# Performance work log

Measured on AMD Instinct MI355X. Metric: run time of the kernel, lower is better.

## Reference

```python
import jax, jax.numpy as jnp
import numpy as np

B, S_SRC, S_TGT = 32, 128, 128
V, E, H = 32000, 256, 256
PAD_ID = 0
NEG = -1.0e9


def setup_inputs() -> dict:
    key = jax.random.key(0)
    ks = jax.random.split(key, 16)
    lengths_de = jax.random.randint(ks[0], (B,), S_SRC // 2, S_SRC + 1)
    idx_de = jax.random.randint(ks[1], (B, S_SRC), 1, V)
    pos = jnp.arange(S_SRC)[None, :]
    indices_de = jnp.where(pos < lengths_de[:, None], idx_de, PAD_ID)
    indices_en = jax.random.randint(ks[2], (B, S_TGT), 1, V)
    lengths_en = jnp.full((B,), S_TGT, dtype=jnp.int32)

    sc = 0.02
    def nrm(k, shape):
        return jax.random.normal(k, shape, dtype=jnp.float32) * sc
    emb_enc = nrm(ks[3], (V, E)).at[PAD_ID].set(0.0)
    emb_dec = nrm(ks[4], (V, E)).at[PAD_ID].set(0.0)
    return {
        "indices_de": indices_de, "lengths_de": lengths_de,
        "indices_en": indices_en, "lengths_en": lengths_en,
        "emb_enc": emb_enc, "emb_dec": emb_dec,
        "W_ih_enc": nrm(ks[5], (H, E)), "W_hh_enc": nrm(ks[6], (H, H)),
        "b_ih_enc": jnp.zeros((H,), jnp.float32), "b_hh_enc": jnp.zeros((H,), jnp.float32),
        "W_ih_dec": nrm(ks[7], (H, E)), "W_hh_dec": nrm(ks[8], (H, H)),
        "b_ih_dec": jnp.zeros((H,), jnp.float32), "b_hh_dec": jnp.zeros((H,), jnp.float32),
        "W_attn": nrm(ks[9], (H, 2 * H)), "b_attn": jnp.zeros((H,), jnp.float32),
        "W_out": nrm(ks[10], (V, H)), "b_out": jnp.zeros((V,), jnp.float32),
    }


def reference(indices_de, lengths_de, indices_en, lengths_en,
              emb_enc, emb_dec,
              W_ih_enc, W_hh_enc, b_ih_enc, b_hh_enc,
              W_ih_dec, W_hh_dec, b_ih_dec, b_hh_dec,
              W_attn, b_attn, W_out, b_out):
    # ---- Encoder: tanh RNN over packed sequence ----
    x_enc = emb_enc[indices_de]                      # [B, S, E]
    valid = jnp.arange(S_SRC)[None, :] < lengths_de[:, None]  # [B, S]

    def enc_step(h, inp):
        x_t, v_t = inp                                # [B,E], [B]
        h_new = jnp.tanh(x_t @ W_ih_enc.T + b_ih_enc + h @ W_hh_enc.T + b_hh_enc)
        h = jnp.where(v_t[:, None], h_new, h)         # frozen past length (pack semantics)
        out = jnp.where(v_t[:, None], h_new, 0.0)     # padded outputs are zero
        return h, out

    h0 = jnp.zeros((B, H), jnp.float32)
    h_final, enc_outs = jax.lax.scan(
        enc_step, h0, (x_enc.transpose(1, 0, 2), valid.T))
    encoder_outputs = enc_outs.transpose(1, 0, 2)     # [B, S, H]
    enc_mask = indices_de == PAD_ID                   # [B, S] True at padding

    # ---- Decoder: per-step RNN cell + dot-product attention + vocab proj ----
    x_dec = emb_dec[indices_en]                       # [B, T, E]

    def dec_step(h, x_t):
        h = jnp.tanh(x_t @ W_ih_dec.T + b_ih_dec + h @ W_hh_dec.T + b_hh_dec)
        scores = jnp.einsum('bh,bsh->bs', h, encoder_outputs)
        scores = jnp.where(enc_mask, NEG, scores)
        attn = jax.nn.softmax(scores, axis=-1)
        context = jnp.einsum('bs,bsh->bh', attn, encoder_outputs)
        combined = jnp.concatenate([context, h], axis=1)          # [B, 2H]
        attn_out = jnp.tanh(combined @ W_attn.T + b_attn)         # [B, H]
        logits_t = attn_out @ W_out.T + b_out                     # [B, V]
        return h, logits_t

    _, logits = jax.lax.scan(dec_step, h_final, x_dec.transpose(1, 0, 2))
    return logits.transpose(1, 0, 2)                  # [B, T, V]
```

## Files before the change

kernel.cpp:

```cpp
#include <hip/hip_runtime.h>
#include <stdint.h>

#define B_ 32
#define S_ 128
#define T_ 128
#define V_ 32000
#define E_ 256
#define H_ 256
#define NEG_ (-1.0e9f)

typedef __attribute__((ext_vector_type(8))) short short8;
typedef __attribute__((ext_vector_type(4))) float floatx4;

__device__ __forceinline__ unsigned short f2bf(float x){
  unsigned u = __float_as_uint(x);
  u = u + 0x7fffu + ((u >> 16) & 1u);
  return (unsigned short)(u >> 16);
}
__device__ __forceinline__ float bf2f(unsigned short s){
  return __uint_as_float(((unsigned)s) << 16);
}
__device__ __forceinline__ float hsum4(float4 v){ return (v.x+v.y)+(v.z+v.w); }
__device__ __forceinline__ void unpack8(uint4 q, float4& lo, float4& hi){
  lo.x = __uint_as_float(q.x << 16); lo.y = __uint_as_float(q.x & 0xffff0000u);
  lo.z = __uint_as_float(q.y << 16); lo.w = __uint_as_float(q.y & 0xffff0000u);
  hi.x = __uint_as_float(q.z << 16); hi.y = __uint_as_float(q.z & 0xffff0000u);
  hi.z = __uint_as_float(q.w << 16); hi.w = __uint_as_float(q.w & 0xffff0000u);
}

#define GLOAD_LDS16(gptr, lptr) \
  __builtin_amdgcn_global_load_lds( \
      (const __attribute__((address_space(1))) unsigned int*)(const void*)(gptr), \
      (__attribute__((address_space(3))) unsigned int*)(void*)(lptr), 16, 0, 0)

#define LDS_BARRIER() do { \
    asm volatile("s_waitcnt lgkmcnt(0)" ::: "memory"); \
    __builtin_amdgcn_s_barrier(); \
  } while(0)

__device__ __forceinline__ void cvt_body(const float* __restrict__ src,
                                         unsigned short* __restrict__ dst,
                                         int blk, int n4){
  int i = blk*256 + (int)threadIdx.x;
  if (i < n4){
    float4 v = ((const float4*)src)[i];
    ushort4 o; o.x=f2bf(v.x); o.y=f2bf(v.y); o.z=f2bf(v.z); o.w=f2bf(v.w);
    ((ushort4*)dst)[i] = o;
  }
}

__device__ __forceinline__ void xih_body(
    const int* __restrict__ idxmat, const float* __restrict__ emb,
    const float* __restrict__ Wih,
    const float* __restrict__ b1, const float* __restrict__ b2,
    float* __restrict__ out, int blk,
    int* idx_s, float4 (*x_s)[64])
{
  int b = blk >> 3;
  int t0 = (blk & 7) << 4;
  int tid = threadIdx.x;
  if (tid < 16) idx_s[tid] = idxmat[b*128 + t0 + tid];
  __syncthreads();
  for (int r = 0; r < 16; ++r)
    ((float*)&x_s[r][0])[tid] = emb[(size_t)idx_s[r]*E_ + tid];
  __syncthreads();
  int j2 = tid & 127, tg = tid >> 7;
  const float4* W0 = (const float4*)(Wih + (size_t)j2*E_);
  const float4* W1 = (const float4*)(Wih + (size_t)(j2+128)*E_);
  float4 a0[8], a1[8];
  #pragma unroll
  for (int t=0;t<8;++t){ a0[t]={0,0,0,0}; a1[t]={0,0,0,0}; }
  for (int e4 = 0; e4 < 64; ++e4){
    float4 w0 = W0[e4], w1 = W1[e4];
    #pragma unroll
    for (int t = 0; t < 8; ++t){
      float4 xv = x_s[tg*8+t][e4];
      a0[t] += w0*xv; a1[t] += w1*xv;
    }
  }
  float bi0 = b1[j2] + b2[j2];
  float bi1 = b1[j2+128] + b2[j2+128];
  #pragma unroll
  for (int t = 0; t < 8; ++t){
    size_t row = (size_t)((b<<7) + t0 + tg*8 + t)*H_;
    out[row + j2]     = hsum4(a0[t]) + bi0;
    out[row + j2+128] = hsum4(a1[t]) + bi1;
  }
}

__global__ __launch_bounds__(256) void k_prep(
    const float* __restrict__ W_out, unsigned short* __restrict__ Wout_bf,
    const float* __restrict__ W_attn, unsigned short* __restrict__ Wattn_bf,
    const int* __restrict__ indices_de, const float* __restrict__ emb_enc,
    const float* __restrict__ W_ih_enc, const float* __restrict__ b_ih_enc,
    const float* __restrict__ b_hh_enc, float* __restrict__ Xih_enc,
    const int* __restrict__ indices_en, const float* __restrict__ emb_dec,
    const float* __restrict__ W_ih_dec, const float* __restrict__ b_ih_dec,
    const float* __restrict__ b_hh_dec, float* __restrict__ Xih_dec)
{
  __shared__ int idx_s[16];
  __shared__ float4 x_s[16][64];
  int bx = blockIdx.x;
  if (bx < 8000){
    cvt_body(W_out, Wout_bf, bx, 2048000);
  } else if (bx < 8128){
    cvt_body(W_attn, Wattn_bf, bx - 8000, 32768);
  } else if (bx < 8384){
    xih_body(indices_de, emb_enc, W_ih_enc, b_ih_enc, b_hh_enc, Xih_enc,
             bx - 8128, idx_s, x_s);
  } else {
    xih_body(indices_en, emb_dec, W_ih_dec, b_ih_dec, b_hh_dec, Xih_dec,
             bx - 8384, idx_s, x_s);
  }
}

__global__ __launch_bounds__(512, 2) void k_rnn2(
    const float* __restrict__ Whh_e, const float* __restrict__ Whh_d,
    const float* __restrict__ Xih_e, const float* __restrict__ Xih_d,
    const int* __restrict__ lengths,
    unsigned short* __restrict__ enc_out,
    float* __restrict__ hseq)
{
  __shared__ float4 h4_s[64];
  __shared__ float part[2][256];
  float* h_s = (float*)h4_s;
  int b = blockIdx.x, tid = threadIdx.x;
  int j = tid & 255, half = tid >> 8;
  float4 w[32];
  const float4* Wr = (const float4*)(Whh_e + (size_t)j*H_ + half*128);
  #pragma unroll
  for (int i = 0; i < 32; ++i) w[i] = Wr[i];
  if (tid < 256) h_s[tid] = 0.f;
  int len = lengths[b];
  __syncthreads();

  for (int t = 0; t < 128; ++t){
    float x = 0.f;
    if (tid < 256) x = Xih_e[(size_t)((b<<7) + t)*H_ + j];
    const float4* hh = h4_s + (half << 5);
    float4 acc0 = {0,0,0,0}, acc1 = {0,0,0,0};
    #pragma unroll
    for (int i = 0; i < 32; i += 2){ acc0 += w[i]*hh[i]; acc1 += w[i+1]*hh[i+1]; }
    part[half][j] = hsum4(acc0) + hsum4(acc1);
    LDS_BARRIER();
    if (tid < 256){
      float s = x + part[0][tid] + part[1][tid];
      float hn = tanhf(s);
      float hold = h_s[tid];
      bool v = (t < len);
      h_s[tid] = v ? hn : hold;
      enc_out[(size_t)((b<<7)+t)*H_ + tid] = f2bf(v ? hn : 0.f);
    }
    LDS_BARRIER();
  }

  Wr = (const float4*)(Whh_d + (size_t)j*H_ + half*128);
  #pragma unroll
  for (int i = 0; i < 32; ++i) w[i] = Wr[i];
  for (int t = 0; t < 128; ++t){
    float x = 0.f;
    if (tid < 256) x = Xih_d[(size_t)((b<<7) + t)*H_ + j];
    const float4* hh = h4_s + (half << 5);
    float4 acc0 = {0,0,0,0}, acc1 = {0,0,0,0};
    #pragma unroll
    for (int i = 0; i < 32; i += 2){ acc0 += w[i]*hh[i]; acc1 += w[i+1]*hh[i+1]; }
    part[half][j] = hsum4(acc0) + hsum4(acc1);
    LDS_BARRIER();
    if (tid < 256){
      float s = x + part[0][tid] + part[1][tid];
      float hn = tanhf(s);
      h_s[tid] = hn;
      hseq[(size_t)((b<<7)+t)*H_ + tid] = hn;
    }
    LDS_BARRIER();
  }
}

__global__ __launch_bounds__(256) void k_attn(
    const unsigned short* __restrict__ enc_out,
    const float* __restrict__ hseq,
    const int* __restrict__ lengths,
    const unsigned short* __restrict__ Wattn,
    const float* __restrict__ battn,
    unsigned short* __restrict__ attn_out)
{
  __shared__ float h_sm[16][256];
  __shared__ float sc[16][132];
  __shared__ float comb[16][512];
  int bx = blockIdx.x; int b = bx >> 3; int t0 = (bx & 7) << 4;
  int tid = threadIdx.x;
  int len = lengths[b];
  for (int r = 0; r < 16; ++r)
    h_sm[r][tid] = hseq[(size_t)((b<<7) + t0 + r)*H_ + tid];
  __syncthreads();
  {
    int s = tid & 127, tg = tid >> 7;
    float4 a[8];
    #pragma unroll
    for (int t=0;t<8;++t) a[t] = {0,0,0,0};
    const uint4* ep = (const uint4*)(enc_out + (size_t)(b*S_ + s)*H_);
    for (int oct = 0; oct < 32; ++oct){
      uint4 q = ep[oct];
      float4 elo, ehi; unpack8(q, elo, ehi);
      #pragma unroll
      for (int t = 0; t < 8; ++t){
        const float4* hp = (const float4*)&h_sm[tg*8+t][oct*8];
        a[t] += elo*hp[0] + ehi*hp[1];
      }
    }
    #pragma unroll
    for (int t = 0; t < 8; ++t)
      sc[tg*8+t][s] = (s < len) ? hsum4(a[t]) : NEG_;
  }
  __syncthreads();
  {
    int wv = tid >> 6, ln = tid & 63;
    for (int r = 0; r < 4; ++r){
      int t = r*4 + wv;
      float v0 = sc[t][ln], v1 = sc[t][ln+64];
      float m = fmaxf(v0, v1);
      #pragma unroll
      for (int off = 32; off >= 1; off >>= 1) m = fmaxf(m, __shfl_xor(m, off));
      float e0 = __expf(v0 - m), e1 = __expf(v1 - m);
      float su = e0 + e1;
      #pragma unroll
      for (int off = 32; off >= 1; off >>= 1) su += __shfl_xor(su, off);
      float inv = 1.0f / su;
      sc[t][ln] = e0*inv; sc[t][ln+64] = e1*inv;
    }
  }
  __syncthreads();
  {
    int hd = tid & 127, tg = tid >> 7;
    float c0[8], c1[8];
    #pragma unroll
    for (int t=0;t<8;++t){ c0[t]=0.f; c1[t]=0.f; }
    for (int s4 = 0; s4 < 32; ++s4){
      float ea[4], eb[4];
      #pragma unroll
      for (int i = 0; i < 4; ++i){
        const unsigned short* er = enc_out + (size_t)(b*S_ + s4*4 + i)*H_;
        ea[i] = bf2f(er[hd]); eb[i] = bf2f(er[hd+128]);
      }
      #pragma unroll
      for (int t = 0; t < 8; ++t){
        float4 av = *(const float4*)&sc[tg*8+t][s4*4];
        c0[t] += av.x*ea[0] + av.y*ea[1] + av.z*ea[2] + av.w*ea[3];
        c1[t] += av.x*eb[0] + av.y*eb[1] + av.z*eb[2] + av.w*eb[3];
      }
    }
    #pragma unroll
    for (int t = 0; t < 8; ++t){
      comb[tg*8+t][hd]     = c0[t];
      comb[tg*8+t][hd+128] = c1[t];
    }
  }
  for (int r = 0; r < 16; ++r) comb[r][256 + tid] = h_sm[r][tid];
  __syncthreads();
  {
    int j2 = tid & 127, tg = tid >> 7;
    float4 a0[8], a1[8];
    #pragma unroll
    for (int t=0;t<8;++t){ a0[t]={0,0,0,0}; a1[t]={0,0,0,0}; }
    const uint4* W0 = (const uint4*)(Wattn + (size_t)j2*512);
    const uint4* W1 = (const uint4*)(Wattn + (size_t)(j2+128)*512);
    for (int oct = 0; oct < 64; ++oct){
      float4 w0lo, w0hi, w1lo, w1hi;
      unpack8(W0[oct], w0lo, w0hi);
      unpack8(W1[oct], w1lo, w1hi);
      #pragma unroll
      for (int t = 0; t < 8; ++t){
        const float4* cp = (const float4*)&comb[tg*8+t][oct*8];
        float4 clo = cp[0], chi = cp[1];
        a0[t] += w0lo*clo + w0hi*chi;
        a1[t] += w1lo*clo + w1hi*chi;
      }
    }
    float bi0 = battn[j2], bi1 = battn[j2+128];
    #pragma unroll
    for (int t = 0; t < 8; ++t){
      size_t row = (size_t)((b<<7) + t0 + tg*8 + t)*H_;
      attn_out[row + j2]     = f2bf(tanhf(hsum4(a0[t]) + bi0));
      attn_out[row + j2+128] = f2bf(tanhf(hsum4(a1[t]) + bi1));
    }
  }
}

__global__ __launch_bounds__(512) void k_vocab(
    const unsigned short* __restrict__ A,
    const unsigned short* __restrict__ Wb,
    const float* __restrict__ bout,
    float* __restrict__ out)
{
  __shared__ alignas(16) unsigned short Asm[2][256*32];
  __shared__ alignas(16) unsigned short Bsm[2][128*32];
  int bid = blockIdx.x;
  int xcd = bid & 7, idx = bid >> 3;
  int nb = idx >> 1;
  int mb = (xcd << 1) | (idx & 1);
  int tid = threadIdx.x;
  int ln  = tid & 63;
  int wid = tid >> 6;
  int llo = ln & 15, lhi = ln >> 4;
  int wr = wid >> 1, wc = wid & 1;
  int mbase = mb*256, nbase = nb*128;

  int ca0 = tid, ca1 = tid + 512, cb = tid;
  int ra0 = ca0 >> 2, sa0 = (ca0 & 3) ^ ((ra0 >> 1) & 3);
  int ra1 = ca1 >> 2, sa1 = (ca1 & 3) ^ ((ra1 >> 1) & 3);
  int rb  = cb  >> 2, sb  = (cb  & 3) ^ ((rb  >> 1) & 3);
  const unsigned short* Ag0 = A  + (size_t)(mbase + ra0)*256 + sa0*8;
  const unsigned short* Ag1 = A  + (size_t)(mbase + ra1)*256 + sa1*8;
  const unsigned short* Bg  = Wb + (size_t)(nbase + rb )*256 + sb*8;

#define STAGE_V(bufi, kk) do { \
    GLOAD_LDS16(Ag0 + (kk), &Asm[bufi][ca0*8]); \
    GLOAD_LDS16(Ag1 + (kk), &Asm[bufi][ca1*8]); \
    GLOAD_LDS16(Bg  + (kk), &Bsm[bufi][cb*8]); \
  } while(0)

  floatx4 acc[4][4];
  #pragma unroll
  for (int mi=0;mi<4;++mi)
    #pragma unroll
    for (int ni=0;ni<4;++ni) acc[mi][ni] = (floatx4){0.f,0.f,0.f,0.f};

  int q = (llo >> 1) & 3;
  int aoff[4], boff[4];
  #pragma unroll
  for (int i=0;i<4;++i){
    aoff[i] = (wr*64 + i*16 + llo)*32 + ((lhi ^ q)*8);
    boff[i] = (wc*64 + i*16 + llo)*32 + ((lhi ^ q)*8);
  }

  STAGE_V(0, 0);
  asm volatile("s_waitcnt vmcnt(0)" ::: "memory");
  __builtin_amdgcn_s_barrier();

  #pragma unroll
  for (int k0 = 0; k0 < 8; ++k0){
    int cur = k0 & 1;
    if (k0 < 7) STAGE_V(cur^1, (k0+1)*32);
    short8 afr[4];
    #pragma unroll
    for (int mi=0;mi<4;++mi)
      afr[mi] = *(const short8*)&Asm[cur][aoff[mi]];
    #pragma unroll
    for (int ni=0;ni<4;++ni){
      short8 bfr = *(const short8*)&Bsm[cur][boff[ni]];
      #pragma unroll
      for (int mi=0;mi<4;++mi)
        acc[mi][ni] = __builtin_amdgcn_mfma_f32_16x16x32_bf16(afr[mi], bfr, acc[mi][ni], 0, 0, 0);
    }
    asm volatile("s_waitcnt vmcnt(0)" ::: "memory");
    __builtin_amdgcn_s_barrier();
  }

  #pragma unroll
  for (int ni = 0; ni < 4; ++ni){
    int col = nbase + wc*64 + ni*16 + llo;
    float bias = bout[col];
    #pragma unroll
    for (int mi = 0; mi < 4; ++mi){
      #pragma unroll
      for (int r = 0; r < 4; ++r){
        int row = mbase + wr*64 + mi*16 + lhi*4 + r;
        out[(size_t)row*V_ + col] = acc[mi][ni][r] + bias;
      }
    }
  }
#undef STAGE_V
}

extern "C" void kernel_launch(void* const* d_in, const int* in_sizes, int n_in,
                              void* d_out, int out_size, void* d_ws, size_t ws_size,
                              hipStream_t stream){
  const int*   indices_de = (const int*)d_in[0];
  const int*   lengths_de = (const int*)d_in[1];
  const int*   indices_en = (const int*)d_in[2];
  const float* emb_enc   = (const float*)d_in[4];
  const float* emb_dec   = (const float*)d_in[5];
  const float* W_ih_enc  = (const float*)d_in[6];
  const float* W_hh_enc  = (const float*)d_in[7];
  const float* b_ih_enc  = (const float*)d_in[8];
  const float* b_hh_enc  = (const float*)d_in[9];
  const float* W_ih_dec  = (const float*)d_in[10];
  const float* W_hh_dec  = (const float*)d_in[11];
  const float* b_ih_dec  = (const float*)d_in[12];
  const float* b_hh_dec  = (const float*)d_in[13];
  const float* W_attn    = (const float*)d_in[14];
  const float* b_attn    = (const float*)d_in[15];
  const float* W_out     = (const float*)d_in[16];
  const float* b_out     = (const float*)d_in[17];

  char* ws = (char*)d_ws;
  size_t o = 0;
  float* Xih_enc = (float*)(ws + o); o += (size_t)4096*256*4;
  float* Xih_dec = (float*)(ws + o); o += (size_t)4096*256*4;
  unsigned short* enc_bf = (unsigned short*)(ws + o); o += (size_t)4096*256*2;
  float* hdec    = (float*)(ws + o); o += (size_t)4096*256*4;
  unsigned short* attn_o  = (unsigned short*)(ws + o); o += (size_t)4096*256*2;
  unsigned short* Wout_bf = (unsigned short*)(ws + o); o += (size_t)V_*256*2;
  unsigned short* Wattn_bf= (unsigned short*)(ws + o); o += (size_t)256*512*2;

  k_prep<<<8640, 256, 0, stream>>>(
      W_out, Wout_bf, W_attn, Wattn_bf,
      indices_de, emb_enc, W_ih_enc, b_ih_enc, b_hh_enc, Xih_enc,
      indices_en, emb_dec, W_ih_dec, b_ih_dec, b_hh_dec, Xih_dec);
  k_rnn2<<<32, 512, 0, stream>>>(W_hh_enc, W_hh_dec, Xih_enc, Xih_dec,
                                 lengths_de, enc_bf, hdec);
  k_attn<<<256, 256, 0, stream>>>(enc_bf, hdec, lengths_de, Wattn_bf, b_attn, attn_o);
  k_vocab<<<4000, 512, 0, stream>>>(attn_o, Wout_bf, b_out, (float*)d_out);
}
```

Baseline: 1.002 ms.

## Split RNN recurrence over 8 k-slices and triple-buffer vocab GEMM loads

The RNN recurrence kernel now splits the 256-wide dot product into 8 k-slices of 32, with each thread computing 4 output rows. Each thread loads its slice of h once into registers and reuses it across those rows, and a reduction over 8 partial sums replaces the previous two-way reduction. The aim is to cut per-thread serial FMA depth and LDS reads on the latency-bound sequential path, at the cost of more LDS partials and a longer final sum. The vocab GEMM moves from double to triple buffering with a prefetch distance of two and waits only for the older loads. This overlaps global-to-LDS copies with MFMA work, but uses more LDS per block and adds an extra barrier per k-step, which may reduce occupancy.

```diff
diff --git a/kernel.cpp b/kernel.cpp
--- a/kernel.cpp
+++ b/kernel.cpp
@@ -121,30 +121,41 @@
     unsigned short* __restrict__ enc_out,
     float* __restrict__ hseq)
 {
-  __shared__ float4 h4_s[64];
-  __shared__ float part[2][256];
-  float* h_s = (float*)h4_s;
+  __shared__ float h_s[256];
+  __shared__ float part[8][256];
   int b = blockIdx.x, tid = threadIdx.x;
-  int j = tid & 255, half = tid >> 8;
-  float4 w[32];
-  const float4* Wr = (const float4*)(Whh_e + (size_t)j*H_ + half*128);
-  #pragma unroll
-  for (int i = 0; i < 32; ++i) w[i] = Wr[i];
+  int kk = tid >> 6;
+  int jg = tid & 63;
+  float4 w[4][8];
+  #pragma unroll
+  for (int r = 0; r < 4; ++r){
+    const float4* Wr = (const float4*)(Whh_e + (size_t)(jg + (r<<6))*H_ + (kk<<5));
+    #pragma unroll
+    for (int i = 0; i < 8; ++i) w[r][i] = Wr[i];
+  }
   if (tid < 256) h_s[tid] = 0.f;
   int len = lengths[b];
   __syncthreads();
 
   for (int t = 0; t < 128; ++t){
     float x = 0.f;
-    if (tid < 256) x = Xih_e[(size_t)((b<<7) + t)*H_ + j];
-    const float4* hh = h4_s + (half << 5);
-    float4 acc0 = {0,0,0,0}, acc1 = {0,0,0,0};
-    #pragma unroll
-    for (int i = 0; i < 32; i += 2){ acc0 += w[i]*hh[i]; acc1 += w[i+1]*hh[i+1]; }
-    part[half][j] = hsum4(acc0) + hsum4(acc1);
+    if (tid < 256) x = Xih_e[(size_t)((b<<7) + t)*H_ + tid];
+    const float4* h4 = ((const float4*)h_s) + (kk << 3);
+    float4 hv[8];
+    #pragma unroll
+    for (int i = 0; i < 8; ++i) hv[i] = h4[i];
+    #pragma unroll
+    for (int r = 0; r < 4; ++r){
+      float4 a = {0,0,0,0};
+      #pragma unroll
+      for (int i = 0; i < 8; ++i) a += w[r][i]*hv[i];
+      part[kk][jg + (r<<6)] = hsum4(a);
+    }
     LDS_BARRIER();
     if (tid < 256){
-      float s = x + part[0][tid] + part[1][tid];
+      float s = x;
+      #pragma unroll
+      for (int q = 0; q < 8; ++q) s += part[q][tid];
       float hn = tanhf(s);
       float hold = h_s[tid];
       bool v = (t < len);
@@ -154,20 +165,31 @@
     LDS_BARRIER();
   }
 
-  Wr = (const float4*)(Whh_d + (size_t)j*H_ + half*128);
-  #pragma unroll
-  for (int i = 0; i < 32; ++i) w[i] = Wr[i];
+  #pragma unroll
+  for (int r = 0; r < 4; ++r){
+    const float4* Wr = (const float4*)(Whh_d + (size_t)(jg + (r<<6))*H_ + (kk<<5));
+    #pragma unroll
+    for (int i = 0; i < 8; ++i) w[r][i] = Wr[i];
+  }
   for (int t = 0; t < 128; ++t){
     float x = 0.f;
-    if (tid < 256) x = Xih_d[(size_t)((b<<7) + t)*H_ + j];
-    const float4* hh = h4_s + (half << 5);
-    float4 acc0 = {0,0,0,0}, acc1 = {0,0,0,0};
-    #pragma unroll
-    for (int i = 0; i < 32; i += 2){ acc0 += w[i]*hh[i]; acc1 += w[i+1]*hh[i+1]; }
-    part[half][j] = hsum4(acc0) + hsum4(acc1);
+    if (tid < 256) x = Xih_d[(size_t)((b<<7) + t)*H_ + tid];
+    const float4* h4 = ((const float4*)h_s) + (kk << 3);
+    float4 hv[8];
+    #pragma unroll
+    for (int i = 0; i < 8; ++i) hv[i] = h4[i];
+    #pragma unroll
+    for (int r = 0; r < 4; ++r){
+      float4 a = {0,0,0,0};
+      #pragma unroll
+      for (int i = 0; i < 8; ++i) a += w[r][i]*hv[i];
+      part[kk][jg + (r<<6)] = hsum4(a);
+    }
     LDS_BARRIER();
     if (tid < 256){
-      float s = x + part[0][tid] + part[1][tid];
+      float s = x;
+      #pragma unroll
+      for (int q = 0; q < 8; ++q) s += part[q][tid];
       float hn = tanhf(s);
       h_s[tid] = hn;
       hseq[(size_t)((b<<7)+t)*H_ + tid] = hn;
@@ -292,8 +314,8 @@
     const float* __restrict__ bout,
     float* __restrict__ out)
 {
-  __shared__ alignas(16) unsigned short Asm[2][256*32];
-  __shared__ alignas(16) unsigned short Bsm[2][128*32];
+  __shared__ alignas(16) unsigned short Asm[3][256*32];
+  __shared__ alignas(16) unsigned short Bsm[3][128*32];
   int bid = blockIdx.x;
   int xcd = bid & 7, idx = bid >> 3;
   int nb = idx >> 1;
@@ -334,26 +356,30 @@
   }
 
   STAGE_V(0, 0);
-  asm volatile("s_waitcnt vmcnt(0)" ::: "memory");
-  __builtin_amdgcn_s_barrier();
+  STAGE_V(1, 32);
 
   #pragma unroll
   for (int k0 = 0; k0 < 8; ++k0){
-    int cur = k0 & 1;
-    if (k0 < 7) STAGE_V(cur^1, (k0+1)*32);
-    short8 afr[4];
-    #pragma unroll
-    for (int mi=0;mi<4;++mi)
-      afr[mi] = *(const short8*)&Asm[cur][aoff[mi]];
-    #pragma unroll
-    for (int ni=0;ni<4;++ni){
-      short8 bfr = *(const short8*)&Bsm[cur][boff[ni]];
+    int cur = k0 % 3;
+    if (k0 < 7) asm volatile("s_waitcnt vmcnt(3)" ::: "memory");
+    else        asm volatile("s_waitcnt vmcnt(0)" ::: "memory");
+    __builtin_amdgcn_s_barrier();
+
+    short8 afr[4], bfr[4];
+    #pragma unroll
+    for (int mi=0;mi<4;++mi) afr[mi] = *(const short8*)&Asm[cur][aoff[mi]];
+    #pragma unroll
+    for (int ni=0;ni<4;++ni) bfr[ni] = *(const short8*)&Bsm[cur][boff[ni]];
+
+    asm volatile("s_waitcnt lgkmcnt(0)" ::: "memory");
+    __builtin_amdgcn_s_barrier();
+    if (k0 < 6) STAGE_V((k0+2)%3, (k0+2)*32);
+
+    #pragma unroll
+    for (int ni=0;ni<4;++ni)
       #pragma unroll
       for (int mi=0;mi<4;++mi)
-        acc[mi][ni] = __builtin_amdgcn_mfma_f32_16x16x32_bf16(afr[mi], bfr, acc[mi][ni], 0, 0, 0);
-    }
-    asm volatile("s_waitcnt vmcnt(0)" ::: "memory");
-    __builtin_amdgcn_s_barrier();
+        acc[mi][ni] = __builtin_amdgcn_mfma_f32_16x16x32_bf16(afr[mi], bfr[ni], acc[mi][ni], 0, 0, 0);
   }
 
   #pragma unroll
```

After: 988.4 us. No clear change (-1.3%).
